# Kernel optimization log

Hardware: AMD Instinct MI355X
Metric: run time of the kernel (lower is better)

The kernel has to match this reference:

```python
import jax, jax.numpy as jnp
import numpy as np

B, T, F, H, NQ = 256, 512, 128, 256, 4


def setup_inputs() -> dict:
    key = jax.random.key(0)
    ks = jax.random.split(key, 7)
    s = 0.1
    return {
        "x": jax.random.normal(ks[0], (B, T, F), dtype=jnp.float32),
        "W_in": jax.random.normal(ks[1], (F + H, NQ), dtype=jnp.float32) * s,
        "b_in": jax.random.normal(ks[2], (NQ,), dtype=jnp.float32) * s,
        "Wq": jax.random.normal(ks[3], (4, NQ, NQ), dtype=jnp.float32) * s,
        "bq": jax.random.normal(ks[4], (4, NQ), dtype=jnp.float32) * s,
        "W_out": jax.random.normal(ks[5], (NQ, H), dtype=jnp.float32) * s,
        "b_out": jax.random.normal(ks[6], (H,), dtype=jnp.float32) * s,
    }


def reference(x, W_in, b_in, Wq, bq, W_out, b_out):
    # x: [B, T, F] (batch_first). Sequential LSTM-like recurrence via lax.scan.
    batch = x.shape[0]
    hidden = W_out.shape[1]

    def step(carry, x_t):
        h, c = carry
        v = jnp.concatenate([h, x_t], axis=1)              # [B, H+F]
        y = v @ W_in + b_in                                # [B, NQ]
        # 4 VQC branches (classical surrogate: tanh(linear)), vectorized over k
        q = jnp.tanh(jnp.einsum('bq,kqr->kbr', y, Wq) + bq[:, None, :])  # [4, B, NQ]
        z = jnp.einsum('kbq,qh->kbh', q, W_out) + b_out    # [4, B, H]
        i = jax.nn.sigmoid(z[0])
        f = jax.nn.sigmoid(z[1])
        g = jnp.tanh(z[2])
        o = jax.nn.sigmoid(z[3])
        c = f * c + i * g
        h = o * jnp.tanh(c)
        return (h, c), h

    h0 = jnp.zeros((batch, hidden), dtype=x.dtype)
    c0 = jnp.zeros((batch, hidden), dtype=x.dtype)
    (h_T, c_T), hs = jax.lax.scan(step, (h0, c0), jnp.swapaxes(x, 0, 1))
    hidden_seq = jnp.swapaxes(hs, 0, 1)                    # [B, T, H]
    return hidden_seq, (h_T, c_T)
```

## Files before the change

### kernel.cpp

```cpp
#include <hip/hip_runtime.h>


#define B_ 256
#define T_ 512
#define F_ 128
#define H_ 256

__device__ __forceinline__ float rcp_f(float x)  { return __builtin_amdgcn_rcpf(x); }
__device__ __forceinline__ float exp2_f(float x) { return __builtin_amdgcn_exp2f(x); }

__device__ __forceinline__ float sigmoid_f(float x) {
    return rcp_f(1.0f + exp2_f(-1.442695041f * x));
}
__device__ __forceinline__ float tanh_f(float x) {
    return 1.0f - 2.0f * rcp_f(1.0f + exp2_f(2.885390082f * x));
}

template<int CTRL>
__device__ __forceinline__ float dpp_add(float v) {
    int p = __builtin_amdgcn_update_dpp(0, __float_as_int(v), CTRL, 0xf, 0xf, true);
    return v + __int_as_float(p);
}

__device__ __forceinline__ float wave_sum63(float v) {
    v = dpp_add<0xB1>(v);
    v = dpp_add<0x4E>(v);
    v = dpp_add<0x141>(v);
    v = dpp_add<0x140>(v);
    v = dpp_add<0x142>(v);
    v = dpp_add<0x143>(v);
    return v;
}

__device__ __forceinline__ void lds_barrier() {
    asm volatile("s_waitcnt lgkmcnt(0)\n\ts_barrier" ::: "memory");
}

__global__ __launch_bounds__(256, 1) void qlstm_kernel(
    const float* __restrict__ x,
    const float* __restrict__ W_in,
    const float* __restrict__ b_in,
    const float* __restrict__ Wq,
    const float* __restrict__ bq,
    const float* __restrict__ W_out,
    const float* __restrict__ b_out,
    float* __restrict__ out)
{
    const int b = blockIdx.x;
    const int g = threadIdx.x;
    const int w = g >> 6;
    const int l = g & 63;

    __shared__ float4 part[2][4];

    const float4* Win4 = (const float4*)W_in;

    float4 t4 = Win4[g];
    float wh[4] = {t4.x, t4.y, t4.z, t4.w};

    const bool has_x = (w < 2);
    float wx[4] = {0.f, 0.f, 0.f, 0.f};
    if (has_x) {
        float4 u4 = Win4[H_ + g];
        wx[0] = u4.x; wx[1] = u4.y; wx[2] = u4.z; wx[3] = u4.w;
    }

    float wo[4];
#pragma unroll
    for (int r = 0; r < 4; ++r) wo[r] = W_out[r * H_ + g];
    const float bo = b_out[g];

    float bin[4];
#pragma unroll
    for (int q = 0; q < 4; ++q) bin[q] = b_in[q];

    const int m = l & 15, qk = m >> 2, qr = m & 3;
    float wql[4];
#pragma unroll
    for (int s = 0; s < 4; ++s) wql[s] = Wq[qk * 16 + s * 4 + qr];
    float bql = bq[qk * 4 + qr];
#pragma unroll
    for (int s = 0; s < 4; ++s) bql = fmaf(bin[s], wql[s], bql);

    float h = 0.f, c = 0.f;

    const float* xp = x + (size_t)b * T_ * F_ + g;
    float xv_next = has_x ? xp[0] : 0.f;

    float* outp = out + (size_t)b * T_ * H_ + g;

    for (int t = 0; t < T_; ++t) {
        const float xv = xv_next;
        if (has_x) {
            int tn = (t + 1 < T_) ? (t + 1) : t;
            xv_next = xp[(size_t)tn * F_];
        }

        float p0 = fmaf(h, wh[0], xv * wx[0]);
        float p1 = fmaf(h, wh[1], xv * wx[1]);
        float p2 = fmaf(h, wh[2], xv * wx[2]);
        float p3 = fmaf(h, wh[3], xv * wx[3]);
        p0 = wave_sum63(p0);
        p1 = wave_sum63(p1);
        p2 = wave_sum63(p2);
        p3 = wave_sum63(p3);
        if (l == 63) part[t & 1][w] = make_float4(p0, p1, p2, p3);
        lds_barrier();
        float4 a0 = part[t & 1][0];
        float4 a1 = part[t & 1][1];
        float4 a2 = part[t & 1][2];
        float4 a3 = part[t & 1][3];
        const float y0 = (a0.x + a1.x) + (a2.x + a3.x);
        const float y1 = (a0.y + a1.y) + (a2.y + a3.y);
        const float y2 = (a0.z + a1.z) + (a2.z + a3.z);
        const float y3 = (a0.w + a1.w) + (a2.w + a3.w);

        float aq = bql;
        aq = fmaf(y0, wql[0], aq);
        aq = fmaf(y1, wql[1], aq);
        aq = fmaf(y2, wql[2], aq);
        aq = fmaf(y3, wql[3], aq);
        const float qown = tanh_f(aq);
        float qs[16];
#pragma unroll
        for (int i = 0; i < 16; ++i)
            qs[i] = __int_as_float(
                __builtin_amdgcn_readlane(__float_as_int(qown), i));

        float z[4];
#pragma unroll
        for (int k = 0; k < 4; ++k) {
            float a = bo;
            a = fmaf(qs[k * 4 + 0], wo[0], a);
            a = fmaf(qs[k * 4 + 1], wo[1], a);
            a = fmaf(qs[k * 4 + 2], wo[2], a);
            a = fmaf(qs[k * 4 + 3], wo[3], a);
            z[k] = a;
        }
        const float ig = sigmoid_f(z[0]);
        const float fg = sigmoid_f(z[1]);
        const float gg = tanh_f(z[2]);
        const float og = sigmoid_f(z[3]);
        c = fmaf(fg, c, ig * gg);
        h = og * tanh_f(c);

        outp[(size_t)t * H_] = h;
    }

    float* hT = out + (size_t)B_ * T_ * H_;
    hT[(size_t)b * H_ + g] = h;
    hT[(size_t)B_ * H_ + (size_t)b * H_ + g] = c;
}

extern "C" void kernel_launch(void* const* d_in, const int* in_sizes, int n_in,
                              void* d_out, int out_size, void* d_ws, size_t ws_size,
                              hipStream_t stream) {
    const float* x     = (const float*)d_in[0];
    const float* W_in  = (const float*)d_in[1];
    const float* b_in  = (const float*)d_in[2];
    const float* Wq    = (const float*)d_in[3];
    const float* bq    = (const float*)d_in[4];
    const float* W_out = (const float*)d_in[5];
    const float* b_out = (const float*)d_in[6];
    float* out = (float*)d_out;

    qlstm_kernel<<<dim3(B_), dim3(256), 0, stream>>>(
        x, W_in, b_in, Wq, bq, W_out, b_out, out);
}
```

Baseline: 394.4 us.

## Collapse each batch row to one wavefront, removing LDS barrier per step

Each block now uses a single 64-lane wavefront that handles four hidden units per lane, so the cross-wave LDS exchange and s_barrier on every timestep are gone and the reduction becomes DPP plus readlane. The FMAs are written as packed two-wide float vectors to map onto packed FP32 instructions. The gate math is fused so sigmoid and tanh share reciprocals. The cost is four times more serial work per lane on the recurrent critical path, with 256 single-wave blocks.

```diff
diff --git a/kernel.cpp b/kernel.cpp
--- a/kernel.cpp
+++ b/kernel.cpp
@@ -6,37 +6,53 @@
 #define F_ 128
 #define H_ 256
 
+typedef float f2 __attribute__((ext_vector_type(2)));
+
 __device__ __forceinline__ float rcp_f(float x)  { return __builtin_amdgcn_rcpf(x); }
 __device__ __forceinline__ float exp2_f(float x) { return __builtin_amdgcn_exp2f(x); }
 
-__device__ __forceinline__ float sigmoid_f(float x) {
-    return rcp_f(1.0f + exp2_f(-1.442695041f * x));
-}
 __device__ __forceinline__ float tanh_f(float x) {
     return 1.0f - 2.0f * rcp_f(1.0f + exp2_f(2.885390082f * x));
 }
 
-template<int CTRL>
-__device__ __forceinline__ float dpp_add(float v) {
-    int p = __builtin_amdgcn_update_dpp(0, __float_as_int(v), CTRL, 0xf, 0xf, true);
-    return v + __int_as_float(p);
+__device__ __forceinline__ f2 splat2(float s) { f2 v; v.x = s; v.y = s; return v; }
+
+__device__ __forceinline__ float rl(float v, int lane) {
+    return __int_as_float(__builtin_amdgcn_readlane(__float_as_int(v), lane));
 }
 
-__device__ __forceinline__ float wave_sum63(float v) {
-    v = dpp_add<0xB1>(v);
-    v = dpp_add<0x4E>(v);
-    v = dpp_add<0x141>(v);
-    v = dpp_add<0x140>(v);
-    v = dpp_add<0x142>(v);
-    v = dpp_add<0x143>(v);
+template<int CTRL>
+__device__ __forceinline__ f2 dpp_add2(f2 v) {
+    int lo = __builtin_amdgcn_update_dpp(0, __float_as_int(v.x), CTRL, 0xf, 0xf, true);
+    int hi = __builtin_amdgcn_update_dpp(0, __float_as_int(v.y), CTRL, 0xf, 0xf, true);
+    f2 p; p.x = __int_as_float(lo); p.y = __int_as_float(hi);
+    return v + p;
+}
+
+__device__ __forceinline__ f2 wave_sum2_63(f2 v) {
+    v = dpp_add2<0xB1>(v);
+    v = dpp_add2<0x4E>(v);
+    v = dpp_add2<0x141>(v);
+    v = dpp_add2<0x140>(v);
+    v = dpp_add2<0x142>(v);
+    v = dpp_add2<0x143>(v);
     return v;
 }
 
-__device__ __forceinline__ void lds_barrier() {
-    asm volatile("s_waitcnt lgkmcnt(0)\n\ts_barrier" ::: "memory");
+__device__ __forceinline__ float lstm_gate(float zi, float zf, float zg, float zo,
+                                           float& c) {
+    const float e0 = exp2_f(-1.442695041f * zi);
+    const float e1 = exp2_f(-1.442695041f * zf);
+    const float E2 = exp2_f( 2.885390082f * zg);
+    const float e3 = exp2_f(-1.442695041f * zo);
+    const float ig = (E2 - 1.0f) * rcp_f((1.0f + e0) * (1.0f + E2));
+    const float fg = rcp_f(1.0f + e1);
+    c = fmaf(fg, c, ig);
+    const float Ec = exp2_f(2.885390082f * c);
+    return (Ec - 1.0f) * rcp_f((1.0f + e3) * (1.0f + Ec));
 }
 
-__global__ __launch_bounds__(256, 1) void qlstm_kernel(
+__global__ __launch_bounds__(64, 1) void qlstm_kernel(
     const float* __restrict__ x,
     const float* __restrict__ W_in,
     const float* __restrict__ b_in,
@@ -47,28 +63,34 @@
     float* __restrict__ out)
 {
     const int b = blockIdx.x;
-    const int g = threadIdx.x;
-    const int w = g >> 6;
-    const int l = g & 63;
-
-    __shared__ float4 part[2][4];
+    const int l = threadIdx.x;
 
     const float4* Win4 = (const float4*)W_in;
 
-    float4 t4 = Win4[g];
-    float wh[4] = {t4.x, t4.y, t4.z, t4.w};
+    f2 wh01[4], wh23[4];
+#pragma unroll
+    for (int k = 0; k < 4; ++k) {
+        float4 r = Win4[4 * l + k];
+        wh01[k].x = r.x; wh01[k].y = r.y;
+        wh23[k].x = r.z; wh23[k].y = r.w;
+    }
+    float4 ra = Win4[H_ + 2 * l];
+    float4 rb = Win4[H_ + 2 * l + 1];
+    f2 wxa01; wxa01.x = ra.x; wxa01.y = ra.y;
+    f2 wxa23; wxa23.x = ra.z; wxa23.y = ra.w;
+    f2 wxb01; wxb01.x = rb.x; wxb01.y = rb.y;
+    f2 wxb23; wxb23.x = rb.z; wxb23.y = rb.w;
 
-    const bool has_x = (w < 2);
-    float wx[4] = {0.f, 0.f, 0.f, 0.f};
-    if (has_x) {
-        float4 u4 = Win4[H_ + g];
-        wx[0] = u4.x; wx[1] = u4.y; wx[2] = u4.z; wx[3] = u4.w;
+    f2 wo01[4], wo23[4];
+#pragma unroll
+    for (int r = 0; r < 4; ++r) {
+        float4 t = *(const float4*)(W_out + r * H_ + 4 * l);
+        wo01[r].x = t.x; wo01[r].y = t.y;
+        wo23[r].x = t.z; wo23[r].y = t.w;
     }
-
-    float wo[4];
-#pragma unroll
-    for (int r = 0; r < 4; ++r) wo[r] = W_out[r * H_ + g];
-    const float bo = b_out[g];
+    float4 bo4 = *(const float4*)(b_out + 4 * l);
+    f2 bo01; bo01.x = bo4.x; bo01.y = bo4.y;
+    f2 bo23; bo23.x = bo4.z; bo23.y = bo4.w;
 
     float bin[4];
 #pragma unroll
@@ -82,38 +104,38 @@
 #pragma unroll
     for (int s = 0; s < 4; ++s) bql = fmaf(bin[s], wql[s], bql);
 
-    float h = 0.f, c = 0.f;
+    float h0 = 0.f, h1 = 0.f, h2 = 0.f, h3 = 0.f;
+    float c0 = 0.f, c1 = 0.f, c2 = 0.f, c3 = 0.f;
 
-    const float* xp = x + (size_t)b * T_ * F_ + g;
-    float xv_next = has_x ? xp[0] : 0.f;
+    const float* xp = x + (size_t)b * T_ * F_ + 2 * l;
+    f2 xv = *(const f2*)xp;
 
-    float* outp = out + (size_t)b * T_ * H_ + g;
+    float4* o4 = (float4*)(out + (size_t)b * T_ * H_) + l;
 
     for (int t = 0; t < T_; ++t) {
-        const float xv = xv_next;
-        if (has_x) {
-            int tn = (t + 1 < T_) ? (t + 1) : t;
-            xv_next = xp[(size_t)tn * F_];
-        }
+        const f2 xc = xv;
+        const int tn = (t + 1 < T_) ? (t + 1) : t;
+        xv = *(const f2*)(xp + (size_t)tn * F_);
 
-        float p0 = fmaf(h, wh[0], xv * wx[0]);
-        float p1 = fmaf(h, wh[1], xv * wx[1]);
-        float p2 = fmaf(h, wh[2], xv * wx[2]);
-        float p3 = fmaf(h, wh[3], xv * wx[3]);
-        p0 = wave_sum63(p0);
-        p1 = wave_sum63(p1);
-        p2 = wave_sum63(p2);
-        p3 = wave_sum63(p3);
-        if (l == 63) part[t & 1][w] = make_float4(p0, p1, p2, p3);
-        lds_barrier();
-        float4 a0 = part[t & 1][0];
-        float4 a1 = part[t & 1][1];
-        float4 a2 = part[t & 1][2];
-        float4 a3 = part[t & 1][3];
-        const float y0 = (a0.x + a1.x) + (a2.x + a3.x);
-        const float y1 = (a0.y + a1.y) + (a2.y + a3.y);
-        const float y2 = (a0.z + a1.z) + (a2.z + a3.z);
-        const float y3 = (a0.w + a1.w) + (a2.w + a3.w);
+        f2 A01 = splat2(xc.x) * wxa01;
+        f2 A23 = splat2(xc.x) * wxa23;
+        f2 B01 = splat2(xc.y) * wxb01;
+        f2 B23 = splat2(xc.y) * wxb23;
+        A01 = splat2(h0) * wh01[0] + A01;
+        A23 = splat2(h0) * wh23[0] + A23;
+        A01 = splat2(h1) * wh01[1] + A01;
+        A23 = splat2(h1) * wh23[1] + A23;
+        B01 = splat2(h2) * wh01[2] + B01;
+        B23 = splat2(h2) * wh23[2] + B23;
+        B01 = splat2(h3) * wh01[3] + B01;
+        B23 = splat2(h3) * wh23[3] + B23;
+
+        f2 s01 = wave_sum2_63(A01 + B01);
+        f2 s23 = wave_sum2_63(A23 + B23);
+        const float y0 = rl(s01.x, 63);
+        const float y1 = rl(s01.y, 63);
+        const float y2 = rl(s23.x, 63);
+        const float y3 = rl(s23.y, 63);
 
         float aq = bql;
         aq = fmaf(y0, wql[0], aq);
@@ -123,33 +145,32 @@
         const float qown = tanh_f(aq);
         float qs[16];
 #pragma unroll
-        for (int i = 0; i < 16; ++i)
-            qs[i] = __int_as_float(
-                __builtin_amdgcn_readlane(__float_as_int(qown), i));
+        for (int i = 0; i < 16; ++i) qs[i] = rl(qown, i);
 
-        float z[4];
+        f2 z01[4] = {bo01, bo01, bo01, bo01};
+        f2 z23[4] = {bo23, bo23, bo23, bo23};
 #pragma unroll
-        for (int k = 0; k < 4; ++k) {
-            float a = bo;
-            a = fmaf(qs[k * 4 + 0], wo[0], a);
-            a = fmaf(qs[k * 4 + 1], wo[1], a);
-            a = fmaf(qs[k * 4 + 2], wo[2], a);
-            a = fmaf(qs[k * 4 + 3], wo[3], a);
-            z[k] = a;
+        for (int r = 0; r < 4; ++r) {
+#pragma unroll
+            for (int k = 0; k < 4; ++k) {
+                const f2 qsp = splat2(qs[k * 4 + r]);
+                z01[k] = qsp * wo01[r] + z01[k];
+                z23[k] = qsp * wo23[r] + z23[k];
+            }
         }
-        const float ig = sigmoid_f(z[0]);
-        const float fg = sigmoid_f(z[1]);
-        const float gg = tanh_f(z[2]);
-        const float og = sigmoid_f(z[3]);
-        c = fmaf(fg, c, ig * gg);
-        h = og * tanh_f(c);
 
-        outp[(size_t)t * H_] = h;
+        h0 = lstm_gate(z01[0].x, z01[1].x, z01[2].x, z01[3].x, c0);
+        h1 = lstm_gate(z01[0].y, z01[1].y, z01[2].y, z01[3].y, c1);
+        h2 = lstm_gate(z23[0].x, z23[1].x, z23[2].x, z23[3].x, c2);
+        h3 = lstm_gate(z23[0].y, z23[1].y, z23[2].y, z23[3].y, c3);
+
+        o4[(size_t)t * (H_ / 4)] = make_float4(h0, h1, h2, h3);
     }
 
     float* hT = out + (size_t)B_ * T_ * H_;
-    hT[(size_t)b * H_ + g] = h;
-    hT[(size_t)B_ * H_ + (size_t)b * H_ + g] = c;
+    *(float4*)(hT + (size_t)b * H_ + 4 * l) = make_float4(h0, h1, h2, h3);
+    *(float4*)(hT + (size_t)B_ * H_ + (size_t)b * H_ + 4 * l) =
+        make_float4(c0, c1, c2, c3);
 }
 
 extern "C" void kernel_launch(void* const* d_in, const int* in_sizes, int n_in,
@@ -164,6 +185,6 @@
     const float* b_out = (const float*)d_in[6];
     float* out = (float*)d_out;
 
-    qlstm_kernel<<<dim3(B_), dim3(256), 0, stream>>>(
+    qlstm_kernel<<<dim3(B_), dim3(64), 0, stream>>>(
         x, W_in, b_in, Wq, bq, W_out, b_out, out);
 }
```

After: 562.3 us. 42.6% more time.

## Fold activation scale constants into weights and merge gate reciprocals

Applied to the files above, without the earlier changes.

Pre-multiplies W_out, b_out, Wq and the input bias by the log2-e scale factors, so each gate's exponent comes straight from the matmul. The cell state is kept in a scaled form C. Reciprocals are combined (i*g and o*tanh(c) each use a single rcp), which cuts transcendental and multiply work on the serial per-step critical path. It also prefetches x two steps ahead and uses packed float2 adds and split FMA chains for more ILP. Combining reciprocals into one product risks overflow or inf for large exponents and changes rounding slightly.

```diff
diff --git a/kernel.cpp b/kernel.cpp
--- a/kernel.cpp
+++ b/kernel.cpp
@@ -6,14 +6,19 @@
 #define F_ 128
 #define H_ 256
 
+#define SC1 1.442695041f
+#define SC2 2.885390082f
+#define ISC2 0.3465735903f
+
+typedef float f2 __attribute__((ext_vector_type(2)));
+
 __device__ __forceinline__ float rcp_f(float x)  { return __builtin_amdgcn_rcpf(x); }
 __device__ __forceinline__ float exp2_f(float x) { return __builtin_amdgcn_exp2f(x); }
 
-__device__ __forceinline__ float sigmoid_f(float x) {
-    return rcp_f(1.0f + exp2_f(-1.442695041f * x));
-}
-__device__ __forceinline__ float tanh_f(float x) {
-    return 1.0f - 2.0f * rcp_f(1.0f + exp2_f(2.885390082f * x));
+__device__ __forceinline__ f2 mk2(float a, float b) { f2 v; v.x = a; v.y = b; return v; }
+
+__device__ __forceinline__ float rl(float v, int lane) {
+    return __int_as_float(__builtin_amdgcn_readlane(__float_as_int(v), lane));
 }
 
 template<int CTRL>
@@ -65,10 +70,20 @@
         wx[0] = u4.x; wx[1] = u4.y; wx[2] = u4.z; wx[3] = u4.w;
     }
 
-    float wo[4];
+    const float sk[4] = {-SC1, -SC1, SC2, -SC1};
+    float wo_k[4][4];
+    float bo_k[4];
+    {
+        const float bo = b_out[g];
 #pragma unroll
-    for (int r = 0; r < 4; ++r) wo[r] = W_out[r * H_ + g];
-    const float bo = b_out[g];
+        for (int r = 0; r < 4; ++r) {
+            const float wor = W_out[r * H_ + g];
+#pragma unroll
+            for (int k = 0; k < 4; ++k) wo_k[k][r] = wor * sk[k];
+        }
+#pragma unroll
+        for (int k = 0; k < 4; ++k) bo_k[k] = bo * sk[k];
+    }
 
     float bin[4];
 #pragma unroll
@@ -81,75 +96,89 @@
     float bql = bq[qk * 4 + qr];
 #pragma unroll
     for (int s = 0; s < 4; ++s) bql = fmaf(bin[s], wql[s], bql);
+    bql *= SC2;
+#pragma unroll
+    for (int s = 0; s < 4; ++s) wql[s] *= SC2;
 
-    float h = 0.f, c = 0.f;
+    float h = 0.f;
+    float C = 0.f;
 
     const float* xp = x + (size_t)b * T_ * F_ + g;
-    float xv_next = has_x ? xp[0] : 0.f;
+    float xb0 = has_x ? xp[0] : 0.f;
+    float xb1 = has_x ? xp[F_] : 0.f;
 
     float* outp = out + (size_t)b * T_ * H_ + g;
 
     for (int t = 0; t < T_; ++t) {
-        const float xv = xv_next;
+        const float xc = xb0;
+        xb0 = xb1;
         if (has_x) {
-            int tn = (t + 1 < T_) ? (t + 1) : t;
-            xv_next = xp[(size_t)tn * F_];
+            int tn = (t + 2 < T_) ? (t + 2) : (T_ - 1);
+            xb1 = xp[(size_t)tn * F_];
         }
 
-        float p0 = fmaf(h, wh[0], xv * wx[0]);
-        float p1 = fmaf(h, wh[1], xv * wx[1]);
-        float p2 = fmaf(h, wh[2], xv * wx[2]);
-        float p3 = fmaf(h, wh[3], xv * wx[3]);
+        const float xq0 = xc * wx[0];
+        const float xq1 = xc * wx[1];
+        const float xq2 = xc * wx[2];
+        const float xq3 = xc * wx[3];
+
+        float p0 = fmaf(h, wh[0], xq0);
+        float p1 = fmaf(h, wh[1], xq1);
+        float p2 = fmaf(h, wh[2], xq2);
+        float p3 = fmaf(h, wh[3], xq3);
         p0 = wave_sum63(p0);
         p1 = wave_sum63(p1);
         p2 = wave_sum63(p2);
         p3 = wave_sum63(p3);
         if (l == 63) part[t & 1][w] = make_float4(p0, p1, p2, p3);
         lds_barrier();
-        float4 a0 = part[t & 1][0];
-        float4 a1 = part[t & 1][1];
-        float4 a2 = part[t & 1][2];
-        float4 a3 = part[t & 1][3];
-        const float y0 = (a0.x + a1.x) + (a2.x + a3.x);
-        const float y1 = (a0.y + a1.y) + (a2.y + a3.y);
-        const float y2 = (a0.z + a1.z) + (a2.z + a3.z);
-        const float y3 = (a0.w + a1.w) + (a2.w + a3.w);
+        const float4 a0 = part[t & 1][0];
+        const float4 a1 = part[t & 1][1];
+        const float4 a2 = part[t & 1][2];
+        const float4 a3 = part[t & 1][3];
+        const f2 y01 = (mk2(a0.x, a0.y) + mk2(a1.x, a1.y)) +
+                       (mk2(a2.x, a2.y) + mk2(a3.x, a3.y));
+        const f2 y23 = (mk2(a0.z, a0.w) + mk2(a1.z, a1.w)) +
+                       (mk2(a2.z, a2.w) + mk2(a3.z, a3.w));
+        const float y0 = y01.x, y1 = y01.y, y2 = y23.x, y3 = y23.y;
 
-        float aq = bql;
-        aq = fmaf(y0, wql[0], aq);
-        aq = fmaf(y1, wql[1], aq);
-        aq = fmaf(y2, wql[2], aq);
-        aq = fmaf(y3, wql[3], aq);
-        const float qown = tanh_f(aq);
+        float u = fmaf(y0, wql[0], bql);
+        const float v = fmaf(y2, wql[2], y1 * wql[1]);
+        u = fmaf(y3, wql[3], u);
+        const float aq = u + v;
+        const float qown = 1.0f - 2.0f * rcp_f(1.0f + exp2_f(aq));
+
         float qs[16];
 #pragma unroll
-        for (int i = 0; i < 16; ++i)
-            qs[i] = __int_as_float(
-                __builtin_amdgcn_readlane(__float_as_int(qown), i));
+        for (int i = 0; i < 16; ++i) qs[i] = rl(qown, i);
 
-        float z[4];
+        float zp[4];
 #pragma unroll
         for (int k = 0; k < 4; ++k) {
-            float a = bo;
-            a = fmaf(qs[k * 4 + 0], wo[0], a);
-            a = fmaf(qs[k * 4 + 1], wo[1], a);
-            a = fmaf(qs[k * 4 + 2], wo[2], a);
-            a = fmaf(qs[k * 4 + 3], wo[3], a);
-            z[k] = a;
+            float a = fmaf(qs[k * 4 + 0], wo_k[k][0], bo_k[k]);
+            const float bsum = fmaf(qs[k * 4 + 1], wo_k[k][1],
+                                    qs[k * 4 + 2] * wo_k[k][2]);
+            a = fmaf(qs[k * 4 + 3], wo_k[k][3], a);
+            zp[k] = a + bsum;
         }
-        const float ig = sigmoid_f(z[0]);
-        const float fg = sigmoid_f(z[1]);
-        const float gg = tanh_f(z[2]);
-        const float og = sigmoid_f(z[3]);
-        c = fmaf(fg, c, ig * gg);
-        h = og * tanh_f(c);
+
+        const float e0 = exp2_f(zp[0]);
+        const float e1 = exp2_f(zp[1]);
+        const float E2 = exp2_f(zp[2]);
+        const float e3 = exp2_f(zp[3]);
+        const float num2 = fmaf(SC2, E2, -SC2);
+        const float IG2  = num2 * rcp_f((1.0f + e0) * (1.0f + E2));
+        const float fg   = rcp_f(1.0f + e1);
+        C = fmaf(fg, C, IG2);
+        const float Ec = exp2_f(C);
+        h = (Ec - 1.0f) * rcp_f((1.0f + e3) * (1.0f + Ec));
 
         outp[(size_t)t * H_] = h;
     }
 
     float* hT = out + (size_t)B_ * T_ * H_;
     hT[(size_t)b * H_ + g] = h;
-    hT[(size_t)B_ * H_ + (size_t)b * H_ + g] = c;
+    hT[(size_t)B_ * H_ + (size_t)b * H_ + g] = C * ISC2;
 }
 
 extern "C" void kernel_launch(void* const* d_in, const int* in_sizes, int n_in,
```

After: 387.5 us. Within noise of the previous version (-1.8%).
